# Optimization experiments

Measured on AMD Instinct MI355X. Metric: run time of the kernel, lower is better.

## Reference

```python
import jax, jax.numpy as jnp
import numpy as np

B, N, N2 = 4, 2048, 1024
DIM, DIM_Y, H = 1024, 1024, 16
HD = DIM // H  # head_dim = 64
SCALE = HD ** -0.5


def setup_inputs() -> dict:
    key = jax.random.key(0)
    ks = jax.random.split(key, 6)
    s = 0.02
    return {
        "x": jax.random.normal(ks[0], (B, N, DIM), dtype=jnp.float32),
        "y": jax.random.normal(ks[1], (B, N2, DIM_Y), dtype=jnp.float32),
        "pad_mask": jax.random.randint(ks[2], (B, N2), 0, 2, dtype=jnp.int32),
        "Wq": jax.random.normal(ks[3], (DIM, DIM), dtype=jnp.float32) * s,
        "Wkv": jax.random.normal(ks[4], (DIM_Y, 2 * DIM), dtype=jnp.float32) * s,
        "Wproj": jax.random.normal(ks[5], (DIM, DIM), dtype=jnp.float32) * s,
        "bproj": jnp.zeros((DIM,), dtype=jnp.float32),
    }


def reference(x, y, pad_mask, Wq, Wkv, Wproj, bproj):
    b, n, c = x.shape
    n2 = y.shape[1]
    # projections (no bias on q/kv, per qkv_bias=False)
    q = (x @ Wq).reshape(b, n, H, HD).transpose(0, 2, 1, 3)          # [B,H,N,HD]
    kv = (y @ Wkv).reshape(b, n2, 2, H, HD).transpose(2, 0, 3, 1, 4)  # [2,B,H,N2,HD]
    k, v = kv[0], kv[1]
    # scaled attention scores with key-side pad mask
    scores = jnp.einsum("bhnd,bhmd->bhnm", q * SCALE, k)             # [B,H,N,N2]
    keep = pad_mask.astype(bool)[:, None, None, :]                   # [B,1,1,N2]
    scores = jnp.where(keep, scores, -jnp.inf)
    attn = jax.nn.softmax(scores, axis=-1)
    out = jnp.einsum("bhnm,bhmd->bhnd", attn, v)                     # [B,H,N,HD]
    out = out.transpose(0, 2, 1, 3).reshape(b, n, c)
    return out @ Wproj + bproj
```

## Files before the change

### kernel.cpp

```cpp
#include <hip/hip_runtime.h>

typedef unsigned short u16;
typedef unsigned int   u32;
typedef unsigned long long u64;
using bf16x8 = __bf16 __attribute__((ext_vector_type(8)));
using f32x4  = float  __attribute__((ext_vector_type(4)));
using f32x16 = float  __attribute__((ext_vector_type(16)));
using u32x2  = u32    __attribute__((ext_vector_type(2)));

#define B_    4
#define N_    2048
#define N2_   1024
#define DIM_  1024
#define H_    16
#define HD_   64
#define SCALE_ 0.125f
#define LOG2E_ 1.4426950408889634f

union PU { u32 w[4]; bf16x8 v; };

__device__ __forceinline__ u16 f2bf(float f) {
  unsigned u = __float_as_uint(f);
  u += 0x7fffu + ((u >> 16) & 1u);
  return (u16)(u >> 16);
}

__device__ __forceinline__ u32 packbf(float lo, float hi) {
  union { __bf16 b[2]; u32 u; } c;
  c.b[0] = (__bf16)lo; c.b[1] = (__bf16)hi;
  return c.u;
}

__device__ __forceinline__ float pair_sum(float x) { return x + __shfl_xor(x, 32); }

__device__ __forceinline__ void gload16(const u16* g, u16* l) {
  __builtin_amdgcn_global_load_lds(
      (const __attribute__((address_space(1))) u32*)g,
      (__attribute__((address_space(3))) u32*)l, 16, 0, 0);
}

__global__ __launch_bounds__(256) void scan_mask(
    const int* __restrict__ pad, int* __restrict__ kidx, int* __restrict__ Nkeep)
{
  const int w = threadIdx.x >> 6, lane = threadIdx.x & 63;
  int base = 0;
#pragma unroll
  for (int c = 0; c < 16; ++c) {
    const int idx = c*64 + lane;
    const int keep = pad[w*N2_ + idx] != 0;
    const u64 m = __ballot(keep);
    const int pre = __popcll(m & ((1ull << lane) - 1ull));
    if (keep) kidx[w*N2_ + base + pre] = idx;
    base += __popcll(m);
  }
  for (int j = base + lane; j < N2_; j += 64) kidx[w*N2_ + j] = 0;
  if (lane == 0) Nkeep[w] = base;
}

__global__ __launch_bounds__(256) void cvt_fused(
    const float* __restrict__ x, const float* __restrict__ y,
    const int* __restrict__ kidx, const int* __restrict__ Nkeep,
    u16* __restrict__ xb, u16* __restrict__ yc)
{
  const int id = blockIdx.x * 256 + threadIdx.x;
  union { u32 w[4]; uint4 u; } c;
  if (id < 1048576) {
    const int i = id * 8;
    const float4 a = *(const float4*)&x[i];
    const float4 b = *(const float4*)&x[i + 4];
    c.w[0] = packbf(a.x, a.y); c.w[1] = packbf(a.z, a.w);
    c.w[2] = packbf(b.x, b.y); c.w[3] = packbf(b.z, b.w);
    *(uint4*)&xb[i] = c.u;
  } else {
    const int e8 = (id - 1048576) * 8;
    const int b   = e8 >> 20;
    const int j   = (e8 >> 10) & 1023;
    const int col = e8 & 1023;
    if (j < Nkeep[b]) {
      const int row = kidx[b*N2_ + j];
      const float* src = &y[((size_t)(b*N2_ + row))*DIM_ + col];
      const float4 a0 = *(const float4*)&src[0];
      const float4 a1 = *(const float4*)&src[4];
      c.w[0] = packbf(a0.x, a0.y); c.w[1] = packbf(a0.z, a0.w);
      c.w[2] = packbf(a1.x, a1.y); c.w[3] = packbf(a1.z, a1.w);
    } else {
      c.w[0] = c.w[1] = c.w[2] = c.w[3] = 0u;
    }
    *(uint4*)&yc[(size_t)(b*N2_ + j)*DIM_ + col] = c.u;
  }
}

__global__ __launch_bounds__(256) void transpose_w_all(
    const float* __restrict__ Wq, const float* __restrict__ Wkv,
    const float* __restrict__ Wproj,
    u16* __restrict__ WqT, u16* __restrict__ WkvT, u16* __restrict__ WprojT)
{
  const int z = blockIdx.z;
  const float* W; u16* Wt; int Nc;
  if      (z == 0) { W = Wq;    Wt = WqT;    Nc = 1024; }
  else if (z == 1) { W = Wkv;   Wt = WkvT;   Nc = 2048; }
  else             { W = Wproj; Wt = WprojT; Nc = 1024; }
  const int n0 = blockIdx.x * 32, k0 = blockIdx.y * 32;
  if (n0 >= Nc) return;
  __shared__ float t[32][33];
  const int tx = threadIdx.x, ty = threadIdx.y;
#pragma unroll
  for (int i = 0; i < 4; ++i)
    t[ty + 8*i][tx] = W[(size_t)(k0 + ty + 8*i) * Nc + n0 + tx];
  __syncthreads();
#pragma unroll
  for (int i = 0; i < 4; ++i)
    Wt[(size_t)(n0 + ty + 8*i) * 1024 + k0 + tx] = f2bf(t[tx][ty + 8*i]);
}

#define GEMM_SHARED                                                            \
  __shared__ __align__(16) u16 As[128 * 64];                                   \
  __shared__ __align__(16) u16 Bs[128 * 64];

#define STAGE(k0) {                                                            \
    _Pragma("unroll")                                                          \
    for (int i = 0; i < 4; ++i) {                                              \
      gload16(ga + (size_t)(8*i)*1024 + (k0), &As[(wave*4 + i) * 512]);        \
      gload16(gb + (size_t)(8*i)*1024 + (k0), &Bs[(wave*4 + i) * 512]);        \
    } }

#define GEMM_BODY(A, Bt, CW)                                                   \
  const int tid = threadIdx.x;                                                 \
  const int lane = tid & 63, wave = tid >> 6;                                  \
  const int wr = wave >> 1, wc = wave & 1;                                     \
  const int lr = lane & 15, lg = lane >> 4;                                    \
  f32x4 acc[4][4] = {};                                                        \
  const int l8 = lane >> 3;                                                    \
  const int c8 = ((lane & 7) ^ l8) * 8;                                        \
  const u16* ga = &A [(size_t)(m0 + 32*wave + l8) * 1024 + c8];                \
  const u16* gb = &Bt[(size_t)(n0 + 32*wave + l8) * 1024 + c8];                \
  for (int t = 0; t < 16; ++t) {                                               \
    STAGE(t * 64);                                                             \
    __syncthreads();                  \
    _Pragma("unroll")                                                          \
    for (int kk = 0; kk < 2; ++kk) {                                           \
      bf16x8 af[4], bfr[4];                                                    \
      _Pragma("unroll")                                                        \
      for (int m = 0; m < 4; ++m) {                                            \
        const int row = wr*64 + m*16 + lr;                                     \
        af[m] = *(const bf16x8*)&As[row*64 + (((kk*4 + lg) ^ (row & 7)) * 8)]; \
      }                                                                        \
      _Pragma("unroll")                                                        \
      for (int n = 0; n < 4; ++n) {                                            \
        const int row = wc*64 + n*16 + lr;                                     \
        bfr[n] = *(const bf16x8*)&Bs[row*64 + (((kk*4 + lg) ^ (row & 7)) * 8)]; \
      }                                                                        \
      __builtin_amdgcn_s_setprio(1);                                           \
      _Pragma("unroll")                                                        \
      for (int m = 0; m < 4; ++m)                                              \
        _Pragma("unroll")                                                      \
        for (int n = 0; n < 4; ++n)                                            \
          acc[m][n] = __builtin_amdgcn_mfma_f32_16x16x32_bf16(af[m], bfr[n], acc[m][n], 0, 0, 0); \
      __builtin_amdgcn_s_setprio(0);                                           \
    }                                                                          \
    __syncthreads();         \
  }                                                                            \
  _Pragma("unroll")                                                            \
  for (int m = 0; m < 4; ++m)                                                  \
    _Pragma("unroll")                                                          \
    for (int n = 0; n < 4; ++n)                                                \
      _Pragma("unroll")                                                        \
      for (int j = 0; j < 4; ++j) {                                            \
        const int r = m0 + wr*64 + m*16 + lg*4 + j;                            \
        const int c = n0 + wc*64 + n*16 + lr;                                  \
        CW;                                                                    \
      }

__global__ __launch_bounds__(256) void gemm3(
    const u16* __restrict__ xb, const u16* __restrict__ yc,
    const u16* __restrict__ WqT, const u16* __restrict__ WkvT,
    const int* __restrict__ Nkeep,
    u16* __restrict__ Qb, u16* __restrict__ Kc, u16* __restrict__ Cvt)
{
  GEMM_SHARED
  const int bx = blockIdx.x;
  if (bx < 512) {
    const int xcd = bx & 7, slot = bx >> 3;
    const int m0 = (xcd*8 + (slot & 7)) * 128;
    const int n0 = (slot >> 3) * 128;
    GEMM_BODY(xb, WqT,
      Qb[(size_t)r * 1024 + c] = f2bf(acc[m][n][j] * (SCALE_*LOG2E_)));
  } else if (bx < 768) {
    const int i = bx - 512;
    const int xcd = i & 7, slot = i >> 3;
    const int m0 = (xcd*4 + (slot & 3)) * 128;
    const int n0 = (slot >> 2) * 128;
    if ((m0 & 1023) >= Nkeep[m0 >> 10]) return;
    GEMM_BODY(yc, WkvT,
      Kc[(size_t)r * 1024 + c] = f2bf(acc[m][n][j]));
  } else {
    const int i = bx - 768;
    const int xcd = i & 7, slot = i >> 3;
    const int m0 = (slot >> 2) * 128;
    const int n0 = (xcd*4 + (slot & 3)) * 128;
    if ((n0 & 1023) >= Nkeep[n0 >> 10]) return;
    const u16* Wv = WkvT + (size_t)1024 * 1024;
    GEMM_BODY(Wv, yc,
      Cvt[(size_t)r * 4096 + c] = f2bf(acc[m][n][j]));
  }
}

__global__ __launch_bounds__(256) void gemm_proj(
    const u16* __restrict__ A, const u16* __restrict__ Bt,
    const float* __restrict__ bias, float* __restrict__ C)
{
  GEMM_SHARED
  const int bx = blockIdx.x;
  const int xcd = bx & 7, slot = bx >> 3;
  const int m0 = (xcd*8 + (slot & 7)) * 128;
  const int n0 = (slot >> 3) * 128;
  GEMM_BODY(A, Bt,
    C[(size_t)r * 1024 + c] = acc[m][n][j] + bias[c]);
}

#define QKSTEP(S, QF, KB) { \
    const int c_ = (((S)*2 + hi) ^ x7) * 8; \
    const bf16x8 ka_ = *(const bf16x8*)&KB[lq*64 + c_]; \
    const bf16x8 kb_ = *(const bf16x8*)&KB[(32+lq)*64 + c_]; \
    s0 = __builtin_amdgcn_mfma_f32_32x32x16_bf16(ka_, QF, s0, 0, 0, 0); \
    s1 = __builtin_amdgcn_mfma_f32_32x32x16_bf16(kb_, QF, s1, 0, 0, 0); }

__global__ __launch_bounds__(512) void attn2(
    const u16* __restrict__ Q, const u16* __restrict__ Kc,
    const u16* __restrict__ Cvt, const int* __restrict__ Nkeep,
    u16* __restrict__ AO)
{
  const int bh = blockIdx.x, qt = blockIdx.y;
  const int b = bh >> 4, h = bh & 15;
  const int tid = threadIdx.x;
  const int wave = tid >> 6, lane = tid & 63;
  const int lq = lane & 31, hi = lane >> 5;
  const int x7 = lq & 7;

  __shared__ __align__(16) u16 Ks[2][64*64];
  __shared__ __align__(16) u16 Vs[2][64*64];
  __shared__ __align__(16) u32 Ps[8][32][36];

  const int nk  = Nkeep[b];
  const int nkr = (nk + 63) & ~63;

  const int qrow = qt*256 + wave*32 + lq;
  const size_t qbase = ((size_t)b*N_ + qrow)*DIM_ + h*HD_;
  const bf16x8 qf0 = *(const bf16x8*)&Q[qbase +  0 + hi*8];
  const bf16x8 qf1 = *(const bf16x8*)&Q[qbase + 16 + hi*8];
  const bf16x8 qf2 = *(const bf16x8*)&Q[qbase + 32 + hi*8];
  const bf16x8 qf3 = *(const bf16x8*)&Q[qbase + 48 + hi*8];

  f32x16 o0 = {}, o1 = {};
  float sacc1 = 0.f;

  const int l8 = lane >> 3;
  const int c8 = ((lane & 7) ^ l8) * 8;
  const u16* gk = &Kc[(size_t)b*N2_*1024 + h*HD_ + (size_t)(8*wave + l8)*1024 + c8];
  const u16* gv = &Cvt[(size_t)(h*HD_ + 8*wave + l8)*4096 + b*N2_ + c8];
  u32 (*pw)[36] = Ps[wave];

#define GSTAGE(buf, kt) { \
    gload16(gk + (size_t)(kt)*1024, &Ks[buf][wave*512]); \
    gload16(gv + (kt),              &Vs[buf][wave*512]); }

  GSTAGE(0, 0);
  __syncthreads();

  int cur = 0;
  for (int kt = 0; kt < nkr; kt += 64) {
    if (kt + 64 < nkr) GSTAGE(cur ^ 1, kt + 64);

    f32x16 s0 = {}, s1 = {};
    if (kt + 64 > nk) {
#pragma unroll
      for (int r = 0; r < 16; ++r) {
        const int key = kt + (r & 3) + 8*(r >> 2) + 4*hi;
        if (key      >= nk) s0[r] = -30000.f;
        if (key + 32 >= nk) s1[r] = -30000.f;
      }
    }

    __builtin_amdgcn_s_setprio(1);
    QKSTEP(0, qf0, Ks[cur]); QKSTEP(1, qf1, Ks[cur]);
    QKSTEP(2, qf2, Ks[cur]); QKSTEP(3, qf3, Ks[cur]);
    __builtin_amdgcn_s_setprio(0);

#pragma unroll
    for (int r = 0; r < 16; ++r) {
      s0[r] = exp2f(s0[r]);
      s1[r] = exp2f(s1[r]);
    }
    {
      f32x16 sm;
#pragma unroll
      for (int r = 0; r < 16; ++r) sm[r] = s0[r] + s1[r];
#pragma unroll
      for (int d = 8; d >= 1; d >>= 1)
#pragma unroll
        for (int r = 0; r < 8; ++r) if (r < d) sm[r] += sm[r + d];
      sacc1 += sm[0];
    }

#pragma unroll
    for (int g = 0; g < 4; ++g) {
      u32x2 wa, wb;
      wa[0] = packbf(s0[4*g+0], s0[4*g+1]);
      wa[1] = packbf(s0[4*g+2], s0[4*g+3]);
      wb[0] = packbf(s1[4*g+0], s1[4*g+1]);
      wb[1] = packbf(s1[4*g+2], s1[4*g+3]);
      *(u32x2*)&pw[lq][     4*g + 2*hi] = wa;
      *(u32x2*)&pw[lq][16 + 4*g + 2*hi] = wb;
    }
    asm volatile("" ::: "memory");

    __builtin_amdgcn_s_setprio(1);
#pragma unroll
    for (int KS = 0; KS < 4; ++KS) {
      PU pu;
#pragma unroll
      for (int j = 0; j < 4; ++j) pu.w[j] = pw[lq][KS*8 + 4*hi + j];
      const int c_ = ((KS*2 + hi) ^ x7) * 8;
      const bf16x8 va = *(const bf16x8*)&Vs[cur][lq*64 + c_];
      const bf16x8 vb = *(const bf16x8*)&Vs[cur][(32+lq)*64 + c_];
      o0 = __builtin_amdgcn_mfma_f32_32x32x16_bf16(va, pu.v, o0, 0, 0, 0);
      o1 = __builtin_amdgcn_mfma_f32_32x32x16_bf16(vb, pu.v, o1, 0, 0, 0);
    }
    __builtin_amdgcn_s_setprio(0);

    __syncthreads();
    cur ^= 1;
  }
#undef GSTAGE

  const float lsum = pair_sum(sacc1);
  const float rls = 1.f / lsum;
  const size_t obase = ((size_t)b*N_ + qrow)*DIM_ + h*HD_;
#pragma unroll
  for (int g = 0; g < 4; ++g) {
    u32x2 w;
    w[0] = packbf(o0[4*g+0]*rls, o0[4*g+1]*rls);
    w[1] = packbf(o0[4*g+2]*rls, o0[4*g+3]*rls);
    *(u32x2*)&AO[obase + 8*g + 4*hi] = w;
    w[0] = packbf(o1[4*g+0]*rls, o1[4*g+1]*rls);
    w[1] = packbf(o1[4*g+2]*rls, o1[4*g+3]*rls);
    *(u32x2*)&AO[obase + 32 + 8*g + 4*hi] = w;
  }
}

extern "C" void kernel_launch(void* const* d_in, const int* in_sizes, int n_in,
                              void* d_out, int out_size, void* d_ws, size_t ws_size,
                              hipStream_t stream)
{
  const float* x     = (const float*)d_in[0];
  const float* y     = (const float*)d_in[1];
  const int*   pad   = (const int*)  d_in[2];
  const float* Wq    = (const float*)d_in[3];
  const float* Wkv   = (const float*)d_in[4];
  const float* Wproj = (const float*)d_in[5];
  const float* bproj = (const float*)d_in[6];

  char* ws = (char*)d_ws;
  u16* Kc     = (u16*)(ws);
  u16* Cvt    = (u16*)(ws + (size_t)( 8<<20));
  u16* yc     = (u16*)(ws + (size_t)(16<<20));
  u16* WqT    = (u16*)(ws + (size_t)(24<<20));
  u16* WkvT   = (u16*)(ws + (size_t)(26<<20));
  u16* WprojT = (u16*)(ws + (size_t)(30<<20));
  u16* Qb     = (u16*)(ws + (size_t)(32<<20));
  u16* AOb    = (u16*)(ws + (size_t)(48<<20));
  u16* xb     = (u16*)d_out;
  int* kidx   = (int*)((char*)d_out + (size_t)(16<<20));
  int* Nkeep  = kidx + B_*N2_;

  const dim3 tb(32, 8);
  scan_mask<<<dim3(1), 256, 0, stream>>>(pad, kidx, Nkeep);
  cvt_fused<<<dim3(6144), 256, 0, stream>>>(x, y, kidx, Nkeep, xb, yc);
  transpose_w_all<<<dim3(64, 32, 3), tb, 0, stream>>>(Wq, Wkv, Wproj,
                                                      WqT, WkvT, WprojT);
  gemm3<<<dim3(1024), 256, 0, stream>>>(xb, yc, WqT, WkvT, Nkeep,
                                        Qb, Kc, Cvt);
  attn2<<<dim3(64, 8), 512, 0, stream>>>(Qb, Kc, Cvt, Nkeep, AOb);
  gemm_proj<<<dim3(512), 256, 0, stream>>>(AOb, WprojT, bproj,
                                           (float*)d_out);
}
```

Measured before the change: 133.8 us.

## Software-pipeline QK of next tile with softmax/PV and fuse prep kernels

The attention loop now computes QK scores for the next key tile before doing exp, pack and PV for the current tile, with K prefetched two tiles ahead and V one tile ahead. This lets matrix-core work overlap the transcendental and pack instructions. The input conversion and weight transpose kernels are merged into one launch to cut launch overhead. Holding two score tiles live raises register pressure and may reduce occupancy.

```diff
diff --git a/kernel.cpp b/kernel.cpp
--- a/kernel.cpp
+++ b/kernel.cpp
@@ -57,60 +57,61 @@
   if (lane == 0) Nkeep[w] = base;
 }
 
-__global__ __launch_bounds__(256) void cvt_fused(
+__global__ __launch_bounds__(256) void prep(
     const float* __restrict__ x, const float* __restrict__ y,
     const int* __restrict__ kidx, const int* __restrict__ Nkeep,
-    u16* __restrict__ xb, u16* __restrict__ yc)
-{
-  const int id = blockIdx.x * 256 + threadIdx.x;
-  union { u32 w[4]; uint4 u; } c;
-  if (id < 1048576) {
-    const int i = id * 8;
-    const float4 a = *(const float4*)&x[i];
-    const float4 b = *(const float4*)&x[i + 4];
-    c.w[0] = packbf(a.x, a.y); c.w[1] = packbf(a.z, a.w);
-    c.w[2] = packbf(b.x, b.y); c.w[3] = packbf(b.z, b.w);
-    *(uint4*)&xb[i] = c.u;
-  } else {
-    const int e8 = (id - 1048576) * 8;
-    const int b   = e8 >> 20;
-    const int j   = (e8 >> 10) & 1023;
-    const int col = e8 & 1023;
-    if (j < Nkeep[b]) {
-      const int row = kidx[b*N2_ + j];
-      const float* src = &y[((size_t)(b*N2_ + row))*DIM_ + col];
-      const float4 a0 = *(const float4*)&src[0];
-      const float4 a1 = *(const float4*)&src[4];
-      c.w[0] = packbf(a0.x, a0.y); c.w[1] = packbf(a0.z, a0.w);
-      c.w[2] = packbf(a1.x, a1.y); c.w[3] = packbf(a1.z, a1.w);
-    } else {
-      c.w[0] = c.w[1] = c.w[2] = c.w[3] = 0u;
-    }
-    *(uint4*)&yc[(size_t)(b*N2_ + j)*DIM_ + col] = c.u;
-  }
-}
-
-__global__ __launch_bounds__(256) void transpose_w_all(
     const float* __restrict__ Wq, const float* __restrict__ Wkv,
     const float* __restrict__ Wproj,
+    u16* __restrict__ xb, u16* __restrict__ yc,
     u16* __restrict__ WqT, u16* __restrict__ WkvT, u16* __restrict__ WprojT)
 {
-  const int z = blockIdx.z;
-  const float* W; u16* Wt; int Nc;
-  if      (z == 0) { W = Wq;    Wt = WqT;    Nc = 1024; }
-  else if (z == 1) { W = Wkv;   Wt = WkvT;   Nc = 2048; }
-  else             { W = Wproj; Wt = WprojT; Nc = 1024; }
-  const int n0 = blockIdx.x * 32, k0 = blockIdx.y * 32;
-  if (n0 >= Nc) return;
   __shared__ float t[32][33];
-  const int tx = threadIdx.x, ty = threadIdx.y;
+  const int bx = blockIdx.x, tid = threadIdx.x;
+  if (bx < 6144) {
+    const int id = bx * 256 + tid;
+    union { u32 w[4]; uint4 u; } c;
+    if (id < 1048576) {
+      const int i = id * 8;
+      const float4 a = *(const float4*)&x[i];
+      const float4 b = *(const float4*)&x[i + 4];
+      c.w[0] = packbf(a.x, a.y); c.w[1] = packbf(a.z, a.w);
+      c.w[2] = packbf(b.x, b.y); c.w[3] = packbf(b.z, b.w);
+      *(uint4*)&xb[i] = c.u;
+    } else {
+      const int e8 = (id - 1048576) * 8;
+      const int b   = e8 >> 20;
+      const int j   = (e8 >> 10) & 1023;
+      const int col = e8 & 1023;
+      if (j < Nkeep[b]) {
+        const int row = kidx[b*N2_ + j];
+        const float* src = &y[((size_t)(b*N2_ + row))*DIM_ + col];
+        const float4 a0 = *(const float4*)&src[0];
+        const float4 a1 = *(const float4*)&src[4];
+        c.w[0] = packbf(a0.x, a0.y); c.w[1] = packbf(a0.z, a0.w);
+        c.w[2] = packbf(a1.x, a1.y); c.w[3] = packbf(a1.z, a1.w);
+      } else {
+        c.w[0] = c.w[1] = c.w[2] = c.w[3] = 0u;
+      }
+      *(uint4*)&yc[(size_t)(b*N2_ + j)*DIM_ + col] = c.u;
+    }
+  } else {
+    const int i = bx - 6144;
+    const int z = i >> 11, rem = i & 2047;
+    const float* W; u16* Wt; int Nc;
+    if      (z == 0) { W = Wq;    Wt = WqT;    Nc = 1024; }
+    else if (z == 1) { W = Wkv;   Wt = WkvT;   Nc = 2048; }
+    else             { W = Wproj; Wt = WprojT; Nc = 1024; }
+    const int n0 = (rem & 63) * 32, k0 = (rem >> 6) * 32;
+    if (n0 >= Nc) return;
+    const int tx = tid & 31, ty = tid >> 5;
 #pragma unroll
-  for (int i = 0; i < 4; ++i)
-    t[ty + 8*i][tx] = W[(size_t)(k0 + ty + 8*i) * Nc + n0 + tx];
-  __syncthreads();
+    for (int ii = 0; ii < 4; ++ii)
+      t[ty + 8*ii][tx] = W[(size_t)(k0 + ty + 8*ii) * Nc + n0 + tx];
+    __syncthreads();
 #pragma unroll
-  for (int i = 0; i < 4; ++i)
-    Wt[(size_t)(n0 + ty + 8*i) * 1024 + k0 + tx] = f2bf(t[tx][ty + 8*i]);
+    for (int ii = 0; ii < 4; ++ii)
+      Wt[(size_t)(n0 + ty + 8*ii) * 1024 + k0 + tx] = f2bf(t[tx][ty + 8*ii]);
+  }
 }
 
 #define GEMM_SHARED                                                            \
@@ -136,7 +137,7 @@
   const u16* gb = &Bt[(size_t)(n0 + 32*wave + l8) * 1024 + c8];                \
   for (int t = 0; t < 16; ++t) {                                               \
     STAGE(t * 64);                                                             \
-    __syncthreads();                  \
+    __syncthreads();                                                           \
     _Pragma("unroll")                                                          \
     for (int kk = 0; kk < 2; ++kk) {                                           \
       bf16x8 af[4], bfr[4];                                                    \
@@ -158,7 +159,7 @@
           acc[m][n] = __builtin_amdgcn_mfma_f32_16x16x32_bf16(af[m], bfr[n], acc[m][n], 0, 0, 0); \
       __builtin_amdgcn_s_setprio(0);                                           \
     }                                                                          \
-    __syncthreads();         \
+    __syncthreads();                                                           \
   }                                                                            \
   _Pragma("unroll")                                                            \
   for (int m = 0; m < 4; ++m)                                                  \
@@ -218,12 +219,60 @@
     C[(size_t)r * 1024 + c] = acc[m][n][j] + bias[c]);
 }
 
-#define QKSTEP(S, QF, KB) { \
-    const int c_ = (((S)*2 + hi) ^ x7) * 8; \
+#define QKSTEP2(S0, S1, SS, QF, KB) { \
+    const int c_ = (((SS)*2 + hi) ^ x7) * 8; \
     const bf16x8 ka_ = *(const bf16x8*)&KB[lq*64 + c_]; \
     const bf16x8 kb_ = *(const bf16x8*)&KB[(32+lq)*64 + c_]; \
-    s0 = __builtin_amdgcn_mfma_f32_32x32x16_bf16(ka_, QF, s0, 0, 0, 0); \
-    s1 = __builtin_amdgcn_mfma_f32_32x32x16_bf16(kb_, QF, s1, 0, 0, 0); }
+    S0 = __builtin_amdgcn_mfma_f32_32x32x16_bf16(ka_, QF, S0, 0, 0, 0); \
+    S1 = __builtin_amdgcn_mfma_f32_32x32x16_bf16(kb_, QF, S1, 0, 0, 0); }
+
+#define QK4(S0, S1, KB) { \
+    QKSTEP2(S0, S1, 0, qf0, KB); QKSTEP2(S0, S1, 1, qf1, KB); \
+    QKSTEP2(S0, S1, 2, qf2, KB); QKSTEP2(S0, S1, 3, qf3, KB); }
+
+#define MASKINIT(S0, S1, KT) { \
+    _Pragma("unroll") \
+    for (int r = 0; r < 16; ++r) { S0[r] = 0.f; S1[r] = 0.f; } \
+    if ((KT) + 64 > nk) { \
+      _Pragma("unroll") \
+      for (int r = 0; r < 16; ++r) { \
+        const int key = (KT) + (r & 3) + 8*(r >> 2) + 4*hi; \
+        if (key      >= nk) S0[r] = -30000.f; \
+        if (key + 32 >= nk) S1[r] = -30000.f; } } }
+
+#define SMPACK(S0, S1) { \
+    _Pragma("unroll") \
+    for (int r = 0; r < 16; ++r) { S0[r] = exp2f(S0[r]); S1[r] = exp2f(S1[r]); } \
+    { f32x16 sm_; \
+      _Pragma("unroll") \
+      for (int r = 0; r < 16; ++r) sm_[r] = S0[r] + S1[r]; \
+      _Pragma("unroll") \
+      for (int d = 8; d >= 1; d >>= 1) \
+        _Pragma("unroll") \
+        for (int r = 0; r < 8; ++r) if (r < d) sm_[r] += sm_[r + d]; \
+      sacc1 += sm_[0]; } \
+    _Pragma("unroll") \
+    for (int g = 0; g < 4; ++g) { \
+      u32x2 wa_, wb_; \
+      wa_[0] = packbf(S0[4*g+0], S0[4*g+1]); wa_[1] = packbf(S0[4*g+2], S0[4*g+3]); \
+      wb_[0] = packbf(S1[4*g+0], S1[4*g+1]); wb_[1] = packbf(S1[4*g+2], S1[4*g+3]); \
+      *(u32x2*)&pw[lq][     4*g + 2*hi] = wa_; \
+      *(u32x2*)&pw[lq][16 + 4*g + 2*hi] = wb_; } \
+    asm volatile("" ::: "memory"); }
+
+#define PVX(VB) { \
+    __builtin_amdgcn_s_setprio(1); \
+    _Pragma("unroll") \
+    for (int KS = 0; KS < 4; ++KS) { \
+      PU pu; \
+      _Pragma("unroll") \
+      for (int j = 0; j < 4; ++j) pu.w[j] = pw[lq][KS*8 + 4*hi + j]; \
+      const int c_ = ((KS*2 + hi) ^ x7) * 8; \
+      const bf16x8 va = *(const bf16x8*)&VB[lq*64 + c_]; \
+      const bf16x8 vb = *(const bf16x8*)&VB[(32+lq)*64 + c_]; \
+      o0 = __builtin_amdgcn_mfma_f32_32x32x16_bf16(va, pu.v, o0, 0, 0, 0); \
+      o1 = __builtin_amdgcn_mfma_f32_32x32x16_bf16(vb, pu.v, o1, 0, 0, 0); } \
+    __builtin_amdgcn_s_setprio(0); }
 
 __global__ __launch_bounds__(512) void attn2(
     const u16* __restrict__ Q, const u16* __restrict__ Kc,
@@ -243,6 +292,7 @@
 
   const int nk  = Nkeep[b];
   const int nkr = (nk + 63) & ~63;
+  const int nt  = nkr >> 6;
 
   const int qrow = qt*256 + wave*32 + lq;
   const size_t qbase = ((size_t)b*N_ + qrow)*DIM_ + h*HD_;
@@ -260,78 +310,43 @@
   const u16* gv = &Cvt[(size_t)(h*HD_ + 8*wave + l8)*4096 + b*N2_ + c8];
   u32 (*pw)[36] = Ps[wave];
 
-#define GSTAGE(buf, kt) { \
-    gload16(gk + (size_t)(kt)*1024, &Ks[buf][wave*512]); \
-    gload16(gv + (kt),              &Vs[buf][wave*512]); }
-
-  GSTAGE(0, 0);
+#define GSK(buf, kt) gload16(gk + (size_t)(kt)*1024, &Ks[buf][wave*512]);
+#define GSV(buf, kt) gload16(gv + (kt),              &Vs[buf][wave*512]);
+
+  GSK(0, 0); GSV(0, 0);
+  if (nt > 1) GSK(1, 64);
   __syncthreads();
 
-  int cur = 0;
-  for (int kt = 0; kt < nkr; kt += 64) {
-    if (kt + 64 < nkr) GSTAGE(cur ^ 1, kt + 64);
-
-    f32x16 s0 = {}, s1 = {};
-    if (kt + 64 > nk) {
-#pragma unroll
-      for (int r = 0; r < 16; ++r) {
-        const int key = kt + (r & 3) + 8*(r >> 2) + 4*hi;
-        if (key      >= nk) s0[r] = -30000.f;
-        if (key + 32 >= nk) s1[r] = -30000.f;
-      }
-    }
-
-    __builtin_amdgcn_s_setprio(1);
-    QKSTEP(0, qf0, Ks[cur]); QKSTEP(1, qf1, Ks[cur]);
-    QKSTEP(2, qf2, Ks[cur]); QKSTEP(3, qf3, Ks[cur]);
-    __builtin_amdgcn_s_setprio(0);
-
-#pragma unroll
-    for (int r = 0; r < 16; ++r) {
-      s0[r] = exp2f(s0[r]);
-      s1[r] = exp2f(s1[r]);
-    }
-    {
-      f32x16 sm;
-#pragma unroll
-      for (int r = 0; r < 16; ++r) sm[r] = s0[r] + s1[r];
-#pragma unroll
-      for (int d = 8; d >= 1; d >>= 1)
-#pragma unroll
-        for (int r = 0; r < 8; ++r) if (r < d) sm[r] += sm[r + d];
-      sacc1 += sm[0];
-    }
-
-#pragma unroll
-    for (int g = 0; g < 4; ++g) {
-      u32x2 wa, wb;
-      wa[0] = packbf(s0[4*g+0], s0[4*g+1]);
-      wa[1] = packbf(s0[4*g+2], s0[4*g+3]);
-      wb[0] = packbf(s1[4*g+0], s1[4*g+1]);
-      wb[1] = packbf(s1[4*g+2], s1[4*g+3]);
-      *(u32x2*)&pw[lq][     4*g + 2*hi] = wa;
-      *(u32x2*)&pw[lq][16 + 4*g + 2*hi] = wb;
-    }
-    asm volatile("" ::: "memory");
-
-    __builtin_amdgcn_s_setprio(1);
-#pragma unroll
-    for (int KS = 0; KS < 4; ++KS) {
-      PU pu;
-#pragma unroll
-      for (int j = 0; j < 4; ++j) pu.w[j] = pw[lq][KS*8 + 4*hi + j];
-      const int c_ = ((KS*2 + hi) ^ x7) * 8;
-      const bf16x8 va = *(const bf16x8*)&Vs[cur][lq*64 + c_];
-      const bf16x8 vb = *(const bf16x8*)&Vs[cur][(32+lq)*64 + c_];
-      o0 = __builtin_amdgcn_mfma_f32_32x32x16_bf16(va, pu.v, o0, 0, 0, 0);
-      o1 = __builtin_amdgcn_mfma_f32_32x32x16_bf16(vb, pu.v, o1, 0, 0, 0);
-    }
-    __builtin_amdgcn_s_setprio(0);
-
-    __syncthreads();
-    cur ^= 1;
-  }
-#undef GSTAGE
+  f32x16 sa0, sa1, sb0, sb1;
+  MASKINIT(sa0, sa1, 0);
+  __builtin_amdgcn_s_setprio(1);
+  QK4(sa0, sa1, Ks[0]);
+  __builtin_amdgcn_s_setprio(0);
+  __syncthreads();
+
+#define TILE(SC0, SC1, SN0, SN1, T) { \
+    const int t_ = (T); \
+    if (t_ + 2 < nt) GSK((t_)&1, (t_+2)*64); \
+    if (t_ + 1 < nt) { \
+      GSV((t_+1)&1, (t_+1)*64); \
+      MASKINIT(SN0, SN1, (t_+1)*64); \
+      __builtin_amdgcn_s_setprio(1); \
+      QK4(SN0, SN1, Ks[(t_+1)&1]); \
+      __builtin_amdgcn_s_setprio(0); } \
+    SMPACK(SC0, SC1); \
+    PVX(Vs[(t_)&1]); \
+    __syncthreads(); \
+  }
+
+  int t = 0;
+  for (; t + 1 < nt; t += 2) {
+    TILE(sa0, sa1, sb0, sb1, t);
+    TILE(sb0, sb1, sa0, sa1, t + 1);
+  }
+  if (t < nt) TILE(sa0, sa1, sb0, sb1, t);
+#undef TILE
+#undef GSK
+#undef GSV
 
   const float lsum = pair_sum(sacc1);
   const float rls = 1.f / lsum;
@@ -373,11 +388,9 @@
   int* kidx   = (int*)((char*)d_out + (size_t)(16<<20));
   int* Nkeep  = kidx + B_*N2_;
 
-  const dim3 tb(32, 8);
   scan_mask<<<dim3(1), 256, 0, stream>>>(pad, kidx, Nkeep);
-  cvt_fused<<<dim3(6144), 256, 0, stream>>>(x, y, kidx, Nkeep, xb, yc);
-  transpose_w_all<<<dim3(64, 32, 3), tb, 0, stream>>>(Wq, Wkv, Wproj,
-                                                      WqT, WkvT, WprojT);
+  prep<<<dim3(12288), 256, 0, stream>>>(x, y, kidx, Nkeep, Wq, Wkv, Wproj,
+                                        xb, yc, WqT, WkvT, WprojT);
   gemm3<<<dim3(1024), 256, 0, stream>>>(xb, yc, WqT, WkvT, Nkeep,
                                         Qb, Kc, Cvt);
   attn2<<<dim3(64, 8), 512, 0, stream>>>(Qb, Kc, Cvt, Nkeep, AOb);
```

After: 136.5 us. +2.1%, slower.
